# Optimization experiments

Measured on AMD Instinct MI355X. Metric: run time of the kernel, lower is better.

The kernel has to match this reference:

```python
import jax, jax.numpy as jnp
import numpy as np

NUM_ITERATIONS = 3
EPS = 1e-8


def squash(s):
    # Hinton squash over the pose dims (last two axes). s: [b, C, os0, os1]
    sq_norm = jnp.sum(s * s, axis=(-2, -1), keepdims=True)
    norm = jnp.sqrt(sq_norm + EPS)
    return (sq_norm / (1.0 + sq_norm)) * (s / norm)


def setup_inputs() -> dict:
    key = jax.random.key(0)
    k1, k2, k3 = jax.random.split(key, 3)
    b, B, H, W = 256, 32, 6, 6
    C, os0, is0 = 10, 16, 16
    input_caps_poses = jax.random.normal(k1, (b, B, H, W, is0, 1), dtype=jnp.float32)
    input_caps_activations = jax.random.uniform(k2, (b, B, H, W), dtype=jnp.float32)
    # weight: [input_caps_types, kh, kw, output_caps_types, os0, is0], std=0.1
    weight = 0.1 * jax.random.normal(k3, (B, H, W, C, os0, is0), dtype=jnp.float32)
    # routing_bias: [C, oh=1, ow=1, os0, os1] initialized to 0.1
    routing_bias = jnp.full((C, 1, 1, os0, 1), 0.1, dtype=jnp.float32)
    return {
        "input_caps_poses": input_caps_poses,
        "input_caps_activations": input_caps_activations,
        "weight": weight,
        "routing_bias": routing_bias,
    }


def reference(input_caps_poses, input_caps_activations, weight, routing_bias):
    # Votes: per input capsule (type B, spatial h,w), transform pose [is0,1]
    # by W[B,h,w,C,os0,is0] -> vote [os0,1] for each output type C.
    # votes: [b, C, B, H, W, os0, os1]
    votes = jnp.einsum('Bhwcoi,bBhwij->bcBhwoj', weight, input_caps_poses)
    b, C, B, H, W, os0, os1 = votes.shape
    bias = routing_bias.reshape(C, os0, os1)  # oh=ow=1

    # Dynamic routing-by-agreement. logits: [b, C, B, H, W]
    logits = jnp.zeros((b, C, B, H, W), dtype=votes.dtype)
    v = None
    c = None
    for it in range(NUM_ITERATIONS):
        c = jax.nn.softmax(logits, axis=1)  # coupling over output types C
        s = jnp.einsum('bcBhw,bcBhwoj->bcoj', c, votes) + bias  # [b,C,os0,os1]
        v = squash(s)
        if it < NUM_ITERATIONS - 1:
            # agreement between output pose and each vote
            logits = logits + jnp.einsum('bcoj,bcBhwoj->bcBhw', v, votes)

    output_caps_poses = v[:, :, None, None]  # [b, C, 1, 1, os0, os1]
    output_caps_activations = jnp.sqrt(
        jnp.sum(v * v, axis=(-2, -1)) + EPS
    )[:, :, None, None]  # [b, C, 1, 1]
    coupling_coefficients = c[:, :, None, None]  # [b, C, 1, 1, B, H, W]
    return (output_caps_poses, output_caps_activations, coupling_coefficients)
```

## Files before the change

kernel.cpp:

```cpp
#include <hip/hip_runtime.h>


#define NPOS 1152
#define NC 10
#define OS 16
#define IS 16
#define NB 256
#define CO (NC * OS)
#define CAPS_EPS 1e-8f
#define PW 6
#define PBLK (NPOS / (4 * PW))
#define PPB (4 * PW)
#define NA2 (NPOS * NC * 64)
#define NB2 (16 * NPOS * 64)
#define VSLD 164

typedef __attribute__((ext_vector_type(4))) short bf16x4;
typedef __attribute__((ext_vector_type(4))) _Float16 halfx4;
typedef __attribute__((ext_vector_type(4))) float floatx4;

#if __has_builtin(__builtin_amdgcn_mfma_f32_16x16x16bf16_1k)
  #define MFMA_KIND 1
#elif __has_builtin(__builtin_amdgcn_mfma_f32_16x16x16f16)
  #define MFMA_KIND 0
#else
  #define MFMA_KIND 2
#endif

__device__ __forceinline__ unsigned f2bf_rne(float x) {
    union { float f; unsigned u; } v; v.f = x;
    return (v.u + 0x7FFFu + ((v.u >> 16) & 1u)) >> 16;
}

__device__ __forceinline__ uint2 pack4(float4 f) {
#if MFMA_KIND != 0
    uint2 r;
    r.x = f2bf_rne(f.x) | (f2bf_rne(f.y) << 16);
    r.y = f2bf_rne(f.z) | (f2bf_rne(f.w) << 16);
    return r;
#else
    union { uint2 u; halfx4 v; } r;
    r.v[0] = (_Float16)f.x; r.v[1] = (_Float16)f.y;
    r.v[2] = (_Float16)f.z; r.v[3] = (_Float16)f.w;
    return r.u;
#endif
}

__device__ __forceinline__ floatx4 MFMA16(uint2 a, uint2 b, floatx4 c) {
#if MFMA_KIND == 1
    union { uint2 u; bf16x4 v; } A, B; A.u = a; B.u = b;
    return __builtin_amdgcn_mfma_f32_16x16x16bf16_1k(A.v, B.v, c, 0, 0, 0);
#elif MFMA_KIND == 0
    union { uint2 u; halfx4 v; } A, B; A.u = a; B.u = b;
    return __builtin_amdgcn_mfma_f32_16x16x16f16(A.v, B.v, c, 0, 0, 0);
#else
    (void)a; (void)b;
    return c;
#endif
}

__global__ __launch_bounds__(256) void preconv2_kernel(
    const float* __restrict__ poses, const float* __restrict__ weight,
    uint2* __restrict__ wsA, uint2* __restrict__ wsB)
{
    const int gid = blockIdx.x * 256 + threadIdx.x;
    if (gid < NA2) {
        const int L = gid & 63, pc = gid >> 6;
        const float4 src = *(const float4*)(weight + (size_t)pc * 256 + (L & 15) * 16 + (L >> 4) * 4);
        wsA[gid] = pack4(src);
    } else {
        const int s = gid - NA2;
        if (s < NB2) {
            const int L = s & 63, bp = s >> 6;
            const int p = bp % NPOS, bt = bp / NPOS;
            const float4 src = *(const float4*)(poses +
                ((size_t)(bt * 16 + (L & 15)) * NPOS + p) * IS + (L >> 4) * 4);
            wsB[s] = pack4(src);
        }
    }
}

template <int IT>
__global__ __launch_bounds__(256) void caps_votes4(
    const uint2* __restrict__ wsA, const uint2* __restrict__ wsB,
    const float* __restrict__ vsum, float* __restrict__ part,
    float* __restrict__ out_coup)
{
    const int t    = threadIdx.x;
    const int wave = t >> 6, lane = t & 63;
    const int bcol = lane & 15, quad = lane >> 4;

    const int n    = blockIdx.x;
    const int xcd  = n & 7, j = n >> 3;
    const int slice = xcd * (PBLK / 8) + (j >> 4);
    const int bt   = j & 15;
    const int b0   = bt * 16;
    const int pbase = slice * PPB + wave * PW;

    __shared__ float s_lds[16 * 161];
    __shared__ float vs_lds[(IT > 0) ? 16 * VSLD : 4];

    for (int k = t; k < 16 * 161; k += 256) s_lds[k] = 0.f;
    if (IT > 0) {
        for (int k = t; k < 16 * CO; k += 256) {
            const int b = k / CO, j2 = k - b * CO;
            vs_lds[b * VSLD + j2] = vsum[(size_t)(b0 + b) * CO + j2];
        }
    }
    __syncthreads();

    floatx4 sacc[NC];
#pragma unroll
    for (int c = 0; c < NC; ++c) sacc[c] = (floatx4)(0.f);

    for (int pi = 0; pi < PW; ++pi) {
        const int p = pbase + pi;
        const uint2* ap = wsA + ((size_t)p * NC) * 64 + lane;
        const uint2 bfrag = wsB[((size_t)bt * NPOS + p) * 64 + lane];

        uint2 af[NC];
#pragma unroll
        for (int c = 0; c < NC; ++c) af[c] = ap[(size_t)c * 64];

        if (IT == 0) {
#pragma unroll
            for (int c = 0; c < NC; ++c) sacc[c] = MFMA16(af[c], bfrag, sacc[c]);
        } else {
            float lg[NC];
            float mx = -1e30f;
#pragma unroll
            for (int c = 0; c < NC; ++c) {
                const floatx4 tmp = MFMA16(af[c], bfrag, (floatx4)(0.f));
                const float4 vsc = *(const float4*)(vs_lds + bcol * VSLD + c * 16 + quad * 4);
                float pt = vsc.x * tmp[0] + vsc.y * tmp[1]
                         + vsc.z * tmp[2] + vsc.w * tmp[3];
                pt += __shfl_xor(pt, 16);
                pt += __shfl_xor(pt, 32);
                lg[c] = pt;
                mx = fmaxf(mx, pt);
            }
            float coup[NC];
            float sum = 0.f;
#pragma unroll
            for (int c = 0; c < NC; ++c) { coup[c] = __expf(lg[c] - mx); sum += coup[c]; }
            const float inv = 1.f / sum;
#pragma unroll
            for (int c = 0; c < NC; ++c) coup[c] *= inv;

            if (IT == 2 && quad == 0) {
                float* cp = out_coup + (size_t)(b0 + bcol) * (NC * NPOS) + p;
#pragma unroll
                for (int c = 0; c < NC; ++c) cp[c * NPOS] = coup[c];
            }

#pragma unroll
            for (int c = 0; c < NC; ++c) {
                const floatx4 tmp = MFMA16(af[c], bfrag, (floatx4)(0.f));
#pragma unroll
                for (int r = 0; r < 4; ++r) sacc[c][r] += coup[c] * tmp[r];
            }
        }
    }

    const float scale = (IT == 0) ? 0.1f : 1.f;
#pragma unroll
    for (int c = 0; c < NC; ++c)
#pragma unroll
        for (int r = 0; r < 4; ++r)
            atomicAdd(&s_lds[bcol * 161 + c * 16 + quad * 4 + r], scale * sacc[c][r]);
    __syncthreads();

    float* pp = part + ((size_t)slice * NB + b0) * CO;
    for (int k = t; k < 16 * CO; k += 256) {
        const int b = k / CO, jj = k - b * CO;
        pp[(size_t)b * CO + jj] = s_lds[b * 161 + jj];
    }
}

__global__ __launch_bounds__(256) void caps_votes_fb(
    const float* __restrict__ poses, const float* __restrict__ weight,
    const float* __restrict__ vsum, float* __restrict__ sbuf,
    float* __restrict__ out_coup, int it)
{
    const int t = threadIdx.x, wave = t >> 6, lane = t & 63;
    const int bcol = lane & 15, quad = lane >> 4;
    const int bt = blockIdx.y, b0 = bt * 16;
    const int pbase = blockIdx.x * PPB + wave * PW;

    __shared__ float s_lds[16 * 161];
    for (int k = t; k < 16 * 161; k += 256) s_lds[k] = 0.f;

    float4 vs[NC];
    if (it > 0) {
        const float* vp = vsum + (size_t)(b0 + bcol) * CO + quad * 4;
#pragma unroll
        for (int c = 0; c < NC; ++c) vs[c] = *(const float4*)(vp + c * 16);
    }
    __syncthreads();

    floatx4 sacc[NC];
#pragma unroll
    for (int c = 0; c < NC; ++c) sacc[c] = (floatx4)(0.f);

    for (int pi = 0; pi < PW; ++pi) {
        const int p = pbase + pi;
        const uint2 bfrag = pack4(*(const float4*)(poses +
            ((size_t)(b0 + bcol) * NPOS + p) * IS + quad * 4));
        floatx4 acc[NC];
#pragma unroll
        for (int c = 0; c < NC; ++c) {
            const uint2 a = pack4(*(const float4*)(weight +
                (size_t)(p * NC + c) * 256 + bcol * 16 + quad * 4));
            acc[c] = MFMA16(a, bfrag, (floatx4)(0.f));
        }
        if (it == 0) {
#pragma unroll
            for (int c = 0; c < NC; ++c)
#pragma unroll
                for (int r = 0; r < 4; ++r) sacc[c][r] += acc[c][r];
        } else {
            float lg[NC], mx = -1e30f;
#pragma unroll
            for (int c = 0; c < NC; ++c) {
                float pt = vs[c].x * acc[c][0] + vs[c].y * acc[c][1]
                         + vs[c].z * acc[c][2] + vs[c].w * acc[c][3];
                pt += __shfl_xor(pt, 16);
                pt += __shfl_xor(pt, 32);
                lg[c] = pt; mx = fmaxf(mx, pt);
            }
            float coup[NC], sum = 0.f;
#pragma unroll
            for (int c = 0; c < NC; ++c) { coup[c] = __expf(lg[c] - mx); sum += coup[c]; }
            const float inv = 1.f / sum;
#pragma unroll
            for (int c = 0; c < NC; ++c) coup[c] *= inv;
            if (it == 2 && quad == 0) {
                float* cp = out_coup + (size_t)(b0 + bcol) * (NC * NPOS) + p;
#pragma unroll
                for (int c = 0; c < NC; ++c) cp[c * NPOS] = coup[c];
            }
#pragma unroll
            for (int c = 0; c < NC; ++c)
#pragma unroll
                for (int r = 0; r < 4; ++r) sacc[c][r] += coup[c] * acc[c][r];
        }
    }

    const float scale = (it == 0) ? 0.1f : 1.f;
#pragma unroll
    for (int c = 0; c < NC; ++c)
#pragma unroll
        for (int r = 0; r < 4; ++r)
            atomicAdd(&s_lds[bcol * 161 + c * 16 + quad * 4 + r], scale * sacc[c][r]);
    __syncthreads();
    for (int k = t; k < 16 * CO; k += 256) {
        const int b = k / CO, jj = k - b * CO;
        unsafeAtomicAdd(&sbuf[(size_t)(b0 + b) * CO + jj], s_lds[b * 161 + jj]);
    }
}

__global__ __launch_bounds__(256) void caps_squash_kernel(
    const float* __restrict__ rbias,
    float* __restrict__ sbuf,
    float* __restrict__ vsum,
    float* __restrict__ out_poses,
    float* __restrict__ out_act,
    int it, int npart)
{
    const int b = blockIdx.x;
    const int t = threadIdx.x;
    if (t >= CO) return;
    const int c = t >> 4;

    const size_t idx = (size_t)b * CO + t;
    float s;
    if (npart > 0) {
        const float* p = sbuf + idx;
        const size_t stride = (size_t)NB * CO;
        float a0 = 0.f, a1 = 0.f, a2 = 0.f, a3 = 0.f;
        int px = 0;
        for (; px + 4 <= npart; px += 4) {
            a0 += p[(size_t)(px + 0) * stride];
            a1 += p[(size_t)(px + 1) * stride];
            a2 += p[(size_t)(px + 2) * stride];
            a3 += p[(size_t)(px + 3) * stride];
        }
        for (; px < npart; ++px) a0 += p[(size_t)px * stride];
        s = ((a0 + a1) + (a2 + a3)) + rbias[t];
    } else {
        s = sbuf[idx] + rbias[t];
    }

    float sq = s * s;
    sq += __shfl_xor(sq, 1);
    sq += __shfl_xor(sq, 2);
    sq += __shfl_xor(sq, 4);
    sq += __shfl_xor(sq, 8);
    const float f = (sq / (1.f + sq)) * rsqrtf(sq + CAPS_EPS);
    const float v = f * s;

    if (it < 2) {
        vsum[idx] += v;
        if (npart == 0) sbuf[idx] = 0.f;
    } else {
        out_poses[idx] = v;
        if ((t & 15) == 0) out_act[(size_t)b * NC + c] = sqrtf(f * f * sq + CAPS_EPS);
    }
}

extern "C" void kernel_launch(void* const* d_in, const int* in_sizes, int n_in,
                              void* d_out, int out_size, void* d_ws, size_t ws_size,
                              hipStream_t stream) {
    const float* poses  = (const float*)d_in[0];
    const float* weight = (const float*)d_in[2];
    const float* rbias  = (const float*)d_in[3];

    float* out       = (float*)d_out;
    float* out_poses = out;
    float* out_act   = out + (size_t)NB * CO;
    float* out_coup  = out_act + (size_t)NB * NC;

    const size_t part_bytes = (size_t)PBLK * NB * CO * sizeof(float);
    const size_t vsum_bytes = (size_t)NB * CO * sizeof(float);
    const size_t frag_bytes = (size_t)(NA2 + NB2) * sizeof(uint2);
    const size_t need_full  = part_bytes + vsum_bytes + frag_bytes;

    if (ws_size >= need_full) {
        float* part = (float*)d_ws;
        float* vsum = part + (size_t)PBLK * NB * CO;
        uint2* wsA  = (uint2*)((char*)d_ws + part_bytes + vsum_bytes);
        uint2* wsB  = wsA + NA2;

        (void)hipMemsetAsync(vsum, 0, vsum_bytes, stream);
        hipLaunchKernelGGL(preconv2_kernel,
                           dim3((NA2 + NB2) / 256), dim3(256), 0, stream,
                           poses, weight, wsA, wsB);

        hipLaunchKernelGGL((caps_votes4<0>), dim3(PBLK * 16), dim3(256), 0, stream,
                           wsA, wsB, vsum, part, out_coup);
        hipLaunchKernelGGL(caps_squash_kernel, dim3(NB), dim3(256), 0, stream,
                           rbias, part, vsum, out_poses, out_act, 0, PBLK);
        hipLaunchKernelGGL((caps_votes4<1>), dim3(PBLK * 16), dim3(256), 0, stream,
                           wsA, wsB, vsum, part, out_coup);
        hipLaunchKernelGGL(caps_squash_kernel, dim3(NB), dim3(256), 0, stream,
                           rbias, part, vsum, out_poses, out_act, 1, PBLK);
        hipLaunchKernelGGL((caps_votes4<2>), dim3(PBLK * 16), dim3(256), 0, stream,
                           wsA, wsB, vsum, part, out_coup);
        hipLaunchKernelGGL(caps_squash_kernel, dim3(NB), dim3(256), 0, stream,
                           rbias, part, vsum, out_poses, out_act, 2, PBLK);
    } else {
        float* sbuf = (float*)d_ws;
        float* vsum = sbuf + (size_t)NB * CO;
        (void)hipMemsetAsync(d_ws, 0, 2 * vsum_bytes, stream);
        for (int it = 0; it < 3; ++it) {
            hipLaunchKernelGGL(caps_votes_fb, dim3(PBLK, 16), dim3(256), 0, stream,
                               poses, weight, vsum, sbuf, out_coup, it);
            hipLaunchKernelGGL(caps_squash_kernel, dim3(NB), dim3(256), 0, stream,
                               rbias, sbuf, vsum, out_poses, out_act, it, 0);
        }
    }
}
```

Before: 283.7 us.

## Materialize bf16 votes once and route from stored votes instead of recomputing

The first kernel now computes the votes with MFMA and stores them in bf16 to a workspace buffer (about 94 MB) while also producing the iteration-0 partial sums. It replaces the pre-pack kernel and the per-iteration MFMA recompute. Routing iterations 1 and 2 run as one kernel per batch item that reads the stored votes, does the softmax and weighted sum, and fuses the squash step. This drops vote recomputation and two squash launches, at the cost of writing the votes once and streaming them twice, plus the extra rounding of votes to bf16.

```diff
diff --git a/kernel.cpp b/kernel.cpp
--- a/kernel.cpp
+++ b/kernel.cpp
@@ -11,9 +11,6 @@
 #define PW 6
 #define PBLK (NPOS / (4 * PW))
 #define PPB (4 * PW)
-#define NA2 (NPOS * NC * 64)
-#define NB2 (16 * NPOS * 64)
-#define VSLD 164
 
 typedef __attribute__((ext_vector_type(4))) short bf16x4;
 typedef __attribute__((ext_vector_type(4))) _Float16 halfx4;
@@ -59,54 +56,33 @@
 #endif
 }
 
-__global__ __launch_bounds__(256) void preconv2_kernel(
+__device__ __forceinline__ float bflo(unsigned u) {
+    union { unsigned x; float f; } v; v.x = u << 16; return v.f;
+}
+__device__ __forceinline__ float bfhi(unsigned u) {
+    union { unsigned x; float f; } v; v.x = u & 0xffff0000u; return v.f;
+}
+__device__ __forceinline__ float bfu(unsigned short u) {
+    union { unsigned x; float f; } v; v.x = ((unsigned)u) << 16; return v.f;
+}
+
+__global__ __launch_bounds__(256) void caps_mat(
     const float* __restrict__ poses, const float* __restrict__ weight,
-    uint2* __restrict__ wsA, uint2* __restrict__ wsB)
-{
-    const int gid = blockIdx.x * 256 + threadIdx.x;
-    if (gid < NA2) {
-        const int L = gid & 63, pc = gid >> 6;
-        const float4 src = *(const float4*)(weight + (size_t)pc * 256 + (L & 15) * 16 + (L >> 4) * 4);
-        wsA[gid] = pack4(src);
-    } else {
-        const int s = gid - NA2;
-        if (s < NB2) {
-            const int L = s & 63, bp = s >> 6;
-            const int p = bp % NPOS, bt = bp / NPOS;
-            const float4 src = *(const float4*)(poses +
-                ((size_t)(bt * 16 + (L & 15)) * NPOS + p) * IS + (L >> 4) * 4);
-            wsB[s] = pack4(src);
-        }
-    }
-}
-
-template <int IT>
-__global__ __launch_bounds__(256) void caps_votes4(
-    const uint2* __restrict__ wsA, const uint2* __restrict__ wsB,
-    const float* __restrict__ vsum, float* __restrict__ part,
-    float* __restrict__ out_coup)
+    unsigned short* __restrict__ votes, float* __restrict__ part)
 {
     const int t    = threadIdx.x;
     const int wave = t >> 6, lane = t & 63;
     const int bcol = lane & 15, quad = lane >> 4;
 
-    const int n    = blockIdx.x;
-    const int xcd  = n & 7, j = n >> 3;
+    const int n     = blockIdx.x;
+    const int xcd   = n & 7, j = n >> 3;
     const int slice = xcd * (PBLK / 8) + (j >> 4);
-    const int bt   = j & 15;
-    const int b0   = bt * 16;
+    const int bt    = j & 15;
+    const int b0    = bt * 16;
     const int pbase = slice * PPB + wave * PW;
 
     __shared__ float s_lds[16 * 161];
-    __shared__ float vs_lds[(IT > 0) ? 16 * VSLD : 4];
-
     for (int k = t; k < 16 * 161; k += 256) s_lds[k] = 0.f;
-    if (IT > 0) {
-        for (int k = t; k < 16 * CO; k += 256) {
-            const int b = k / CO, j2 = k - b * CO;
-            vs_lds[b * VSLD + j2] = vsum[(size_t)(b0 + b) * CO + j2];
-        }
-    }
     __syncthreads();
 
     floatx4 sacc[NC];
@@ -115,59 +91,31 @@
 
     for (int pi = 0; pi < PW; ++pi) {
         const int p = pbase + pi;
-        const uint2* ap = wsA + ((size_t)p * NC) * 64 + lane;
-        const uint2 bfrag = wsB[((size_t)bt * NPOS + p) * 64 + lane];
-
-        uint2 af[NC];
-#pragma unroll
-        for (int c = 0; c < NC; ++c) af[c] = ap[(size_t)c * 64];
-
-        if (IT == 0) {
-#pragma unroll
-            for (int c = 0; c < NC; ++c) sacc[c] = MFMA16(af[c], bfrag, sacc[c]);
-        } else {
-            float lg[NC];
-            float mx = -1e30f;
-#pragma unroll
-            for (int c = 0; c < NC; ++c) {
-                const floatx4 tmp = MFMA16(af[c], bfrag, (floatx4)(0.f));
-                const float4 vsc = *(const float4*)(vs_lds + bcol * VSLD + c * 16 + quad * 4);
-                float pt = vsc.x * tmp[0] + vsc.y * tmp[1]
-                         + vsc.z * tmp[2] + vsc.w * tmp[3];
-                pt += __shfl_xor(pt, 16);
-                pt += __shfl_xor(pt, 32);
-                lg[c] = pt;
-                mx = fmaxf(mx, pt);
-            }
-            float coup[NC];
-            float sum = 0.f;
-#pragma unroll
-            for (int c = 0; c < NC; ++c) { coup[c] = __expf(lg[c] - mx); sum += coup[c]; }
-            const float inv = 1.f / sum;
-#pragma unroll
-            for (int c = 0; c < NC; ++c) coup[c] *= inv;
-
-            if (IT == 2 && quad == 0) {
-                float* cp = out_coup + (size_t)(b0 + bcol) * (NC * NPOS) + p;
-#pragma unroll
-                for (int c = 0; c < NC; ++c) cp[c * NPOS] = coup[c];
-            }
-
-#pragma unroll
-            for (int c = 0; c < NC; ++c) {
-                const floatx4 tmp = MFMA16(af[c], bfrag, (floatx4)(0.f));
-#pragma unroll
-                for (int r = 0; r < 4; ++r) sacc[c][r] += coup[c] * tmp[r];
-            }
-        }
-    }
-
-    const float scale = (IT == 0) ? 0.1f : 1.f;
+        const uint2 bfrag = pack4(*(const float4*)(poses +
+            ((size_t)(b0 + bcol) * NPOS + p) * IS + quad * 4));
+
+        float4 ar[NC];
+#pragma unroll
+        for (int c = 0; c < NC; ++c)
+            ar[c] = *(const float4*)(weight +
+                ((size_t)p * NC + c) * 256 + bcol * 16 + quad * 4);
+
+#pragma unroll
+        for (int c = 0; c < NC; ++c) {
+            const uint2 af = pack4(ar[c]);
+            const floatx4 tmp = MFMA16(af, bfrag, (floatx4)(0.f));
+            const size_t vidx = (((size_t)(b0 + bcol) * NC + c) * NPOS + p) * 16 + quad * 4;
+            float4 tf; tf.x = tmp[0]; tf.y = tmp[1]; tf.z = tmp[2]; tf.w = tmp[3];
+            *(uint2*)(votes + vidx) = pack4(tf);
+            sacc[c] = sacc[c] + tmp;
+        }
+    }
+
 #pragma unroll
     for (int c = 0; c < NC; ++c)
 #pragma unroll
         for (int r = 0; r < 4; ++r)
-            atomicAdd(&s_lds[bcol * 161 + c * 16 + quad * 4 + r], scale * sacc[c][r]);
+            atomicAdd(&s_lds[bcol * 161 + c * 16 + quad * 4 + r], 0.1f * sacc[c][r]);
     __syncthreads();
 
     float* pp = part + ((size_t)slice * NB + b0) * CO;
@@ -177,85 +125,109 @@
     }
 }
 
-__global__ __launch_bounds__(256) void caps_votes_fb(
-    const float* __restrict__ poses, const float* __restrict__ weight,
-    const float* __restrict__ vsum, float* __restrict__ sbuf,
-    float* __restrict__ out_coup, int it)
+template <int ITX>
+__global__ __launch_bounds__(512) void caps_route(
+    const unsigned short* __restrict__ votes,
+    const float* __restrict__ rbias,
+    float* __restrict__ vsum,
+    float* __restrict__ out_coup,
+    float* __restrict__ out_poses,
+    float* __restrict__ out_act)
 {
-    const int t = threadIdx.x, wave = t >> 6, lane = t & 63;
-    const int bcol = lane & 15, quad = lane >> 4;
-    const int bt = blockIdx.y, b0 = bt * 16;
-    const int pbase = blockIdx.x * PPB + wave * PW;
-
-    __shared__ float s_lds[16 * 161];
-    for (int k = t; k < 16 * 161; k += 256) s_lds[k] = 0.f;
-
-    float4 vs[NC];
-    if (it > 0) {
-        const float* vp = vsum + (size_t)(b0 + bcol) * CO + quad * 4;
-#pragma unroll
-        for (int c = 0; c < NC; ++c) vs[c] = *(const float4*)(vp + c * 16);
-    }
-    __syncthreads();
-
-    floatx4 sacc[NC];
-#pragma unroll
-    for (int c = 0; c < NC; ++c) sacc[c] = (floatx4)(0.f);
-
-    for (int pi = 0; pi < PW; ++pi) {
-        const int p = pbase + pi;
-        const uint2 bfrag = pack4(*(const float4*)(poses +
-            ((size_t)(b0 + bcol) * NPOS + p) * IS + quad * 4));
-        floatx4 acc[NC];
+    const int b = blockIdx.x;
+    const int t = threadIdx.x;
+
+    __shared__ float v_lds[CO];
+    __shared__ float coup_lds[NPOS * NC];
+    __shared__ float s_part[3 * 168];
+
+    if (t < CO) v_lds[t] = vsum[(size_t)b * CO + t];
+    __syncthreads();
+
+    const int nk = (t < NPOS - 1024) ? 3 : 2;
+    for (int k = 0; k < nk; ++k) {
+        const int p = t + 512 * k;
+        const size_t pb16 = ((size_t)b * NC * NPOS + p) * 16;
+
+        float lg[NC];
 #pragma unroll
         for (int c = 0; c < NC; ++c) {
-            const uint2 a = pack4(*(const float4*)(weight +
-                (size_t)(p * NC + c) * 256 + bcol * 16 + quad * 4));
-            acc[c] = MFMA16(a, bfrag, (floatx4)(0.f));
-        }
-        if (it == 0) {
-#pragma unroll
-            for (int c = 0; c < NC; ++c)
-#pragma unroll
-                for (int r = 0; r < 4; ++r) sacc[c][r] += acc[c][r];
+            const uint4* vp = (const uint4*)(votes + pb16 + (size_t)c * (NPOS * 16));
+            const uint4 u0 = vp[0];
+            const uint4 u1 = vp[1];
+            const float* vl = v_lds + c * 16;
+            float a = 0.f;
+            a = fmaf(bflo(u0.x), vl[0],  a); a = fmaf(bfhi(u0.x), vl[1],  a);
+            a = fmaf(bflo(u0.y), vl[2],  a); a = fmaf(bfhi(u0.y), vl[3],  a);
+            a = fmaf(bflo(u0.z), vl[4],  a); a = fmaf(bfhi(u0.z), vl[5],  a);
+            a = fmaf(bflo(u0.w), vl[6],  a); a = fmaf(bfhi(u0.w), vl[7],  a);
+            a = fmaf(bflo(u1.x), vl[8],  a); a = fmaf(bfhi(u1.x), vl[9],  a);
+            a = fmaf(bflo(u1.y), vl[10], a); a = fmaf(bfhi(u1.y), vl[11], a);
+            a = fmaf(bflo(u1.z), vl[12], a); a = fmaf(bfhi(u1.z), vl[13], a);
+            a = fmaf(bflo(u1.w), vl[14], a); a = fmaf(bfhi(u1.w), vl[15], a);
+            lg[c] = a;
+        }
+        float mx = lg[0];
+#pragma unroll
+        for (int c = 1; c < NC; ++c) mx = fmaxf(mx, lg[c]);
+        float coup[NC];
+        float sum = 0.f;
+#pragma unroll
+        for (int c = 0; c < NC; ++c) { coup[c] = __expf(lg[c] - mx); sum += coup[c]; }
+        const float inv = 1.f / sum;
+#pragma unroll
+        for (int c = 0; c < NC; ++c) {
+            coup[c] *= inv;
+            coup_lds[p * NC + c] = coup[c];
+        }
+        if (ITX == 2) {
+            float* cp = out_coup + (size_t)b * (NC * NPOS) + p;
+#pragma unroll
+            for (int c = 0; c < NC; ++c) cp[(size_t)c * NPOS] = coup[c];
+        }
+    }
+    __syncthreads();
+
+    if (t < 480) {
+        const int co  = t % 160;
+        const int seg = t / 160;
+        const int c = co >> 4, o = co & 15;
+        const unsigned short* vp = votes + ((size_t)b * NC + c) * (NPOS * 16) + o;
+        const float* cl = coup_lds + c;
+        const int p0 = seg * 384;
+        float a0 = 0.f, a1 = 0.f, a2 = 0.f, a3 = 0.f;
+        for (int p = p0; p < p0 + 384; p += 8) {
+            a0 = fmaf(cl[(p + 0) * NC], bfu(vp[(size_t)(p + 0) * 16]), a0);
+            a1 = fmaf(cl[(p + 1) * NC], bfu(vp[(size_t)(p + 1) * 16]), a1);
+            a2 = fmaf(cl[(p + 2) * NC], bfu(vp[(size_t)(p + 2) * 16]), a2);
+            a3 = fmaf(cl[(p + 3) * NC], bfu(vp[(size_t)(p + 3) * 16]), a3);
+            a0 = fmaf(cl[(p + 4) * NC], bfu(vp[(size_t)(p + 4) * 16]), a0);
+            a1 = fmaf(cl[(p + 5) * NC], bfu(vp[(size_t)(p + 5) * 16]), a1);
+            a2 = fmaf(cl[(p + 6) * NC], bfu(vp[(size_t)(p + 6) * 16]), a2);
+            a3 = fmaf(cl[(p + 7) * NC], bfu(vp[(size_t)(p + 7) * 16]), a3);
+        }
+        s_part[seg * 168 + co] = ((a0 + a1) + (a2 + a3));
+    }
+    __syncthreads();
+
+    if (t < CO) {
+        const int c = t >> 4;
+        const float s = s_part[0 * 168 + t] + s_part[1 * 168 + t]
+                      + s_part[2 * 168 + t] + rbias[t];
+        float sq = s * s;
+        sq += __shfl_xor(sq, 1);
+        sq += __shfl_xor(sq, 2);
+        sq += __shfl_xor(sq, 4);
+        sq += __shfl_xor(sq, 8);
+        const float f = (sq / (1.f + sq)) * rsqrtf(sq + CAPS_EPS);
+        const float v = f * s;
+        const size_t idx = (size_t)b * CO + t;
+        if (ITX == 1) {
+            vsum[idx] += v;
         } else {
-            float lg[NC], mx = -1e30f;
-#pragma unroll
-            for (int c = 0; c < NC; ++c) {
-                float pt = vs[c].x * acc[c][0] + vs[c].y * acc[c][1]
-                         + vs[c].z * acc[c][2] + vs[c].w * acc[c][3];
-                pt += __shfl_xor(pt, 16);
-                pt += __shfl_xor(pt, 32);
-                lg[c] = pt; mx = fmaxf(mx, pt);
-            }
-            float coup[NC], sum = 0.f;
-#pragma unroll
-            for (int c = 0; c < NC; ++c) { coup[c] = __expf(lg[c] - mx); sum += coup[c]; }
-            const float inv = 1.f / sum;
-#pragma unroll
-            for (int c = 0; c < NC; ++c) coup[c] *= inv;
-            if (it == 2 && quad == 0) {
-                float* cp = out_coup + (size_t)(b0 + bcol) * (NC * NPOS) + p;
-#pragma unroll
-                for (int c = 0; c < NC; ++c) cp[c * NPOS] = coup[c];
-            }
-#pragma unroll
-            for (int c = 0; c < NC; ++c)
-#pragma unroll
-                for (int r = 0; r < 4; ++r) sacc[c][r] += coup[c] * acc[c][r];
-        }
-    }
-
-    const float scale = (it == 0) ? 0.1f : 1.f;
-#pragma unroll
-    for (int c = 0; c < NC; ++c)
-#pragma unroll
-        for (int r = 0; r < 4; ++r)
-            atomicAdd(&s_lds[bcol * 161 + c * 16 + quad * 4 + r], scale * sacc[c][r]);
-    __syncthreads();
-    for (int k = t; k < 16 * CO; k += 256) {
-        const int b = k / CO, jj = k - b * CO;
-        unsafeAtomicAdd(&sbuf[(size_t)(b0 + b) * CO + jj], s_lds[b * 161 + jj]);
+            out_poses[idx] = v;
+            if ((t & 15) == 0) out_act[(size_t)b * NC + c] = sqrtf(f * f * sq + CAPS_EPS);
+        }
     }
 }
 
@@ -308,6 +280,88 @@
     }
 }
 
+__global__ __launch_bounds__(256) void caps_votes_fb(
+    const float* __restrict__ poses, const float* __restrict__ weight,
+    const float* __restrict__ vsum, float* __restrict__ sbuf,
+    float* __restrict__ out_coup, int it)
+{
+    const int t = threadIdx.x, wave = t >> 6, lane = t & 63;
+    const int bcol = lane & 15, quad = lane >> 4;
+    const int bt = blockIdx.y, b0 = bt * 16;
+    const int pbase = blockIdx.x * PPB + wave * PW;
+
+    __shared__ float s_lds[16 * 161];
+    for (int k = t; k < 16 * 161; k += 256) s_lds[k] = 0.f;
+
+    float4 vs[NC];
+    if (it > 0) {
+        const float* vp = vsum + (size_t)(b0 + bcol) * CO + quad * 4;
+#pragma unroll
+        for (int c = 0; c < NC; ++c) vs[c] = *(const float4*)(vp + c * 16);
+    }
+    __syncthreads();
+
+    floatx4 sacc[NC];
+#pragma unroll
+    for (int c = 0; c < NC; ++c) sacc[c] = (floatx4)(0.f);
+
+    for (int pi = 0; pi < PW; ++pi) {
+        const int p = pbase + pi;
+        const uint2 bfrag = pack4(*(const float4*)(poses +
+            ((size_t)(b0 + bcol) * NPOS + p) * IS + quad * 4));
+        floatx4 acc[NC];
+#pragma unroll
+        for (int c = 0; c < NC; ++c) {
+            const uint2 a = pack4(*(const float4*)(weight +
+                (size_t)(p * NC + c) * 256 + bcol * 16 + quad * 4));
+            acc[c] = MFMA16(a, bfrag, (floatx4)(0.f));
+        }
+        if (it == 0) {
+#pragma unroll
+            for (int c = 0; c < NC; ++c)
+#pragma unroll
+                for (int r = 0; r < 4; ++r) sacc[c][r] += acc[c][r];
+        } else {
+            float lg[NC], mx = -1e30f;
+#pragma unroll
+            for (int c = 0; c < NC; ++c) {
+                float pt = vs[c].x * acc[c][0] + vs[c].y * acc[c][1]
+                         + vs[c].z * acc[c][2] + vs[c].w * acc[c][3];
+                pt += __shfl_xor(pt, 16);
+                pt += __shfl_xor(pt, 32);
+                lg[c] = pt; mx = fmaxf(mx, pt);
+            }
+            float coup[NC], sum = 0.f;
+#pragma unroll
+            for (int c = 0; c < NC; ++c) { coup[c] = __expf(lg[c] - mx); sum += coup[c]; }
+            const float inv = 1.f / sum;
+#pragma unroll
+            for (int c = 0; c < NC; ++c) coup[c] *= inv;
+            if (it == 2 && quad == 0) {
+                float* cp = out_coup + (size_t)(b0 + bcol) * (NC * NPOS) + p;
+#pragma unroll
+                for (int c = 0; c < NC; ++c) cp[c * NPOS] = coup[c];
+            }
+#pragma unroll
+            for (int c = 0; c < NC; ++c)
+#pragma unroll
+                for (int r = 0; r < 4; ++r) sacc[c][r] += coup[c] * acc[c][r];
+        }
+    }
+
+    const float scale = (it == 0) ? 0.1f : 1.f;
+#pragma unroll
+    for (int c = 0; c < NC; ++c)
+#pragma unroll
+        for (int r = 0; r < 4; ++r)
+            atomicAdd(&s_lds[bcol * 161 + c * 16 + quad * 4 + r], scale * sacc[c][r]);
+    __syncthreads();
+    for (int k = t; k < 16 * CO; k += 256) {
+        const int b = k / CO, jj = k - b * CO;
+        unsafeAtomicAdd(&sbuf[(size_t)(b0 + b) * CO + jj], s_lds[b * 161 + jj]);
+    }
+}
+
 extern "C" void kernel_launch(void* const* d_in, const int* in_sizes, int n_in,
                               void* d_out, int out_size, void* d_ws, size_t ws_size,
                               hipStream_t stream) {
@@ -320,34 +374,26 @@
     float* out_act   = out + (size_t)NB * CO;
     float* out_coup  = out_act + (size_t)NB * NC;
 
-    const size_t part_bytes = (size_t)PBLK * NB * CO * sizeof(float);
-    const size_t vsum_bytes = (size_t)NB * CO * sizeof(float);
-    const size_t frag_bytes = (size_t)(NA2 + NB2) * sizeof(uint2);
-    const size_t need_full  = part_bytes + vsum_bytes + frag_bytes;
+    const size_t part_bytes  = (size_t)PBLK * NB * CO * sizeof(float);
+    const size_t vsum_bytes  = (size_t)NB * CO * sizeof(float);
+    const size_t votes_bytes = (size_t)NB * NC * NPOS * 16 * sizeof(unsigned short);
+    const size_t need_full   = part_bytes + vsum_bytes + votes_bytes;
 
     if (ws_size >= need_full) {
         float* part = (float*)d_ws;
         float* vsum = part + (size_t)PBLK * NB * CO;
-        uint2* wsA  = (uint2*)((char*)d_ws + part_bytes + vsum_bytes);
-        uint2* wsB  = wsA + NA2;
+        unsigned short* votes = (unsigned short*)((char*)d_ws + part_bytes + vsum_bytes);
 
         (void)hipMemsetAsync(vsum, 0, vsum_bytes, stream);
-        hipLaunchKernelGGL(preconv2_kernel,
-                           dim3((NA2 + NB2) / 256), dim3(256), 0, stream,
-                           poses, weight, wsA, wsB);
-
-        hipLaunchKernelGGL((caps_votes4<0>), dim3(PBLK * 16), dim3(256), 0, stream,
-                           wsA, wsB, vsum, part, out_coup);
+
+        hipLaunchKernelGGL(caps_mat, dim3(PBLK * 16), dim3(256), 0, stream,
+                           poses, weight, votes, part);
         hipLaunchKernelGGL(caps_squash_kernel, dim3(NB), dim3(256), 0, stream,
                            rbias, part, vsum, out_poses, out_act, 0, PBLK);
-        hipLaunchKernelGGL((caps_votes4<1>), dim3(PBLK * 16), dim3(256), 0, stream,
-                           wsA, wsB, vsum, part, out_coup);
-        hipLaunchKernelGGL(caps_squash_kernel, dim3(NB), dim3(256), 0, stream,
-                           rbias, part, vsum, out_poses, out_act, 1, PBLK);
-        hipLaunchKernelGGL((caps_votes4<2>), dim3(PBLK * 16), dim3(256), 0, stream,
-                           wsA, wsB, vsum, part, out_coup);
-        hipLaunchKernelGGL(caps_squash_kernel, dim3(NB), dim3(256), 0, stream,
-                           rbias, part, vsum, out_poses, out_act, 2, PBLK);
+        hipLaunchKernelGGL((caps_route<1>), dim3(NB), dim3(512), 0, stream,
+                           votes, rbias, vsum, out_coup, out_poses, out_act);
+        hipLaunchKernelGGL((caps_route<2>), dim3(NB), dim3(512), 0, stream,
+                           votes, rbias, vsum, out_coup, out_poses, out_act);
     } else {
         float* sbuf = (float*)d_ws;
         float* vsum = sbuf + (size_t)NB * CO;
```

Measured after the change: 271.0 us. 4.5% less time.
